# Kernel optimization log

Measured on AMD Instinct MI355X. Metric: run time of the kernel, lower is better.

The kernel has to match this reference:

```python
import jax, jax.numpy as jnp
import numpy as np

B = 65536          # number of 9-node graphs
NPG = 9            # nodes per graph (hardcoded in module)
N = B * NPG
D_IN, D_H = 11, 64
SOFTPLUS_BIAS = float(np.log(np.expm1(1.0)))  # biased_softplus_1.0 bias
SCALE_LB = 1e-4


def _make_edges():
    # fully connected (no self loops) within each 9-node graph
    pairs = np.array([(i, j) for i in range(NPG) for j in range(NPG) if i != j],
                     dtype=np.int64)  # [72, 2]
    offs = (np.arange(B, dtype=np.int64) * NPG)[:, None]
    src = (offs + pairs[None, :, 0]).ravel()
    dst = (offs + pairs[None, :, 1]).ravel()
    return jnp.asarray(np.stack([src, dst]))  # [2, E]


def setup_inputs() -> dict:
    key = jax.random.key(0)
    ks = jax.random.split(key, 12)
    s_in = 1.0 / np.sqrt(D_IN)
    s_h = 1.0 / np.sqrt(D_H)
    return {
        "x": jax.random.normal(ks[0], (N, D_IN), jnp.float32),
        "edge_index": _make_edges(),
        "W_in": jax.random.normal(ks[1], (D_H, D_IN), jnp.float32) * s_in,
        "b_in": jax.random.normal(ks[2], (D_H,), jnp.float32) * s_in,
        "W1_rel": jax.random.normal(ks[3], (D_H, D_H), jnp.float32) * s_h,
        "b1": jax.random.normal(ks[4], (D_H,), jnp.float32) * s_h,
        "W1_root": jax.random.normal(ks[5], (D_H, D_H), jnp.float32) * s_h,
        "W2_rel": jax.random.normal(ks[6], (D_H, D_H), jnp.float32) * s_h,
        "b2": jax.random.normal(ks[7], (D_H,), jnp.float32) * s_h,
        "W2_root": jax.random.normal(ks[8], (D_H, D_H), jnp.float32) * s_h,
        "W_head": jax.random.normal(ks[9], (8, D_H, 2), jnp.float32) * s_h,
        "b_head": jax.random.normal(ks[10], (8, 2), jnp.float32) * s_h,
    }


def _graph_conv(x, src, dst, W_rel, b_rel, W_root, n):
    # PyG GraphConv: lin_rel(sum_{j in N(i)} x_j) + lin_root(x_i)
    agg = jax.ops.segment_sum(x[src], dst, num_segments=n)  # scatter-add gather
    return agg @ W_rel.T + b_rel + x @ W_root.T


def reference(x, edge_index, W_in, b_in, W1_rel, b1, W1_root,
              W2_rel, b2, W2_root, W_head, b_head):
    n = x.shape[0]
    src, dst = edge_index[0], edge_index[1]
    h = x @ W_in.T + b_in                                   # [N, 64]
    h = jnp.tanh(_graph_conv(h, src, dst, W1_rel, b1, W1_root, n))
    h = jnp.tanh(_graph_conv(h, src, dst, W2_rel, b2, W2_root, n))
    hg = h.reshape(n // NPG, NPG, D_H)[:, 1:, :]            # drop node 0: [B, 8, 64]
    out = jnp.einsum('bnd,ndo->bno', hg, W_head) + b_head   # per-node head: [B, 8, 2]
    loc = out[..., 0]
    scale = jnp.maximum(jax.nn.softplus(out[..., 1] + SOFTPLUS_BIAS), SCALE_LB)
    return (loc, scale)
```

## Files before the change

### kernel.cpp

```cpp
#include <hip/hip_runtime.h>
#include <hip/hip_bf16.h>

#define NPG 9
#define DH 64
#define DIN 11
#define GPB 16
#define TPW 4
#define TPB 256
#define NGRAPH 65536
#define NBLK (NGRAPH/GPB)
#define XTOT (NGRAPH*NPG*DIN)
#define OUT_HALF ((long long)NGRAPH*8)

typedef __attribute__((ext_vector_type(8))) short short8;
typedef __attribute__((ext_vector_type(4))) float f32x4;

__device__ float g_c1[DH];
__device__ short g_bfrag1[8*512];
__device__ short g_bfrag2[16*512];
__device__ short g_bfragH[2*512];

__device__ __forceinline__ short f2bs(float f) {
  __hip_bfloat16 h = __float2bfloat16(f);
  return __builtin_bit_cast(short, h);
}
__device__ __forceinline__ float fast_tanh(float v) {
  float e = __expf(2.f*v);
  return 1.f - 2.f*__builtin_amdgcn_rcpf(e + 1.f);
}

__global__ void prep_kernel(const float* __restrict__ W_in, const float* __restrict__ b_in,
                            const float* __restrict__ W1_rel, const float* __restrict__ b1,
                            const float* __restrict__ W1_root,
                            const float* __restrict__ W2_rel, const float* __restrict__ W2_root,
                            const float* __restrict__ W_head) {
  const int blk = blockIdx.x, tid = threadIdx.x;
  if (blk < 2) {
    for (int i = blk*256 + tid; i < 8*512; i += 512) {
      int f = i >> 9, l = (i >> 3) & 63, j = i & 7;
      int k = ((l >> 4) << 3) + j;
      int n = ((f & 3) << 4) + (l & 15);
      float v = 0.f;
      if (k < DIN) {
        for (int m = 0; m < DH; ++m) {
          float wi = W_in[m*DIN + k];
          float r  = W1_rel[n*DH + m];
          v += ((f < 4) ? (W1_root[n*DH + m] - r) : r) * wi;
        }
      }
      g_bfrag1[i] = f2bs(v);
    }
  } else if (blk < 10) {
    for (int i = (blk - 2)*256 + tid; i < 16*512; i += 2048) {
      int frag = i >> 9, kk = frag >> 2;
      int l = (i >> 3) & 63, j = i & 7;
      int k2 = kk*32 + ((l >> 4) << 3) + j;
      int n  = (frag & 3)*16 + (l & 15);
      float v = (k2 < 64) ? (W2_root[n*DH + k2] - W2_rel[n*DH + k2])
                          : W2_rel[n*DH + k2 - 64];
      g_bfrag2[i] = f2bs(v);
    }
  } else if (blk == 10) {
    for (int i = tid; i < 2*512; i += 256) {
      int kk = i >> 9;
      int l = (i >> 3) & 63, j = i & 7;
      int k = kk*32 + ((l >> 4) << 3) + j;
      int n = l & 15;
      g_bfragH[i] = f2bs(W_head[(n >> 1)*(DH*2) + k*2 + (n & 1)]);
    }
  } else {
    if (tid < DH) {
      float c = b1[tid];
      for (int m = 0; m < DH; ++m)
        c += (W1_root[tid*DH + m] + 8.f*W1_rel[tid*DH + m]) * b_in[m];
      g_c1[tid] = c;
    }
  }
}

__global__ __launch_bounds__(TPB, 2) void fused_kernel(
    const float* __restrict__ x,
    const float* __restrict__ b2,
    const float* __restrict__ bhead,
    float* __restrict__ out)
{
  __shared__ short Hs[256*64];
  __shared__ short Ss[GPB*64];

  const int tid  = threadIdx.x;
  const int lane = tid & 63;
  const int wave = tid >> 6;
  const int l15  = lane & 15;
  const int kgrp = lane >> 4;
  const int ksel = kgrp & 1;
  const int t0   = wave*TPW;
  const unsigned gg0 = (unsigned)blockIdx.x*GPB + t0;

  {
    short8 By[4], Bu[4];
    #pragma unroll
    for (int nt = 0; nt < 4; ++nt) {
      By[nt] = *(const short8*)&g_bfrag1[nt*512 + lane*8];
      Bu[nt] = *(const short8*)&g_bfrag1[(4 + nt)*512 + lane*8];
    }
    float c1v[4];
    #pragma unroll
    for (int nt = 0; nt < 4; ++nt) c1v[nt] = g_c1[nt*16 + l15];

    float xr[TPW][8];
    #pragma unroll
    for (int i = 0; i < TPW; ++i) {
      const unsigned base = ((gg0 + i)*NPG + l15)*DIN + ksel*8;
      if (base + 8 <= (unsigned)XTOT) {
        #pragma unroll
        for (int j = 0; j < 8; ++j) xr[i][j] = x[base + j];
      } else {
        #pragma unroll
        for (int j = 0; j < 8; ++j) {
          const unsigned e = base + j;
          xr[i][j] = (e < (unsigned)XTOT) ? x[e] : 0.f;
        }
      }
    }

    const bool real = (l15 <= 8);
    #pragma unroll
    for (int i = 0; i < TPW; ++i) {
      const int T = t0 + i;
      short8 A;
      #pragma unroll
      for (int j = 0; j < 8; ++j) {
        bool ok = real && (ksel == 0 || j < 3);
        A[j] = ok ? f2bs(xr[i][j]) : (short)0;
      }
      f32x4 y[4], u[4];
      #pragma unroll
      for (int nt = 0; nt < 4; ++nt) { y[nt] = (f32x4){0,0,0,0}; u[nt] = (f32x4){0,0,0,0}; }
      #pragma unroll
      for (int nt = 0; nt < 4; ++nt) {
        y[nt] = __builtin_amdgcn_mfma_f32_16x16x32_bf16(A, By[nt], y[nt], 0, 0, 0);
        u[nt] = __builtin_amdgcn_mfma_f32_16x16x32_bf16(A, Bu[nt], u[nt], 0, 0, 0);
      }
      float suc[4];
      #pragma unroll
      for (int nt = 0; nt < 4; ++nt) {
        float s = (u[nt][0] + u[nt][1]) + (u[nt][2] + u[nt][3]);
        s += __shfl_xor(s, 16);
        s += __shfl_xor(s, 32);
        suc[nt] = s + c1v[nt];
      }
      float sh[4];
      #pragma unroll
      for (int nt = 0; nt < 4; ++nt) {
        float acc = 0.f;
        #pragma unroll
        for (int reg = 0; reg < 4; ++reg) {
          const int row = kgrp*4 + reg;
          float v = fast_tanh(y[nt][reg] + suc[nt]);
          v = (row <= 8) ? v : 0.f;
          acc += v;
          const int rr  = T*16 + row;
          const int col = nt*16 + l15;
          Hs[rr*64 + ((((col >> 3) ^ (row & 7))) << 3) + (col & 7)] = f2bs(v);
        }
        sh[nt] = acc;
      }
      #pragma unroll
      for (int nt = 0; nt < 4; ++nt) {
        float s = sh[nt];
        s += __shfl_xor(s, 16);
        s += __shfl_xor(s, 32);
        if (kgrp == 0) Ss[T*64 + nt*16 + l15] = f2bs(s);
      }
    }
  }

  {
    short8 B2[4][4];
    #pragma unroll
    for (int kk = 0; kk < 4; ++kk)
      #pragma unroll
      for (int nt = 0; nt < 4; ++nt)
        B2[kk][nt] = *(const short8*)&g_bfrag2[(kk*4 + nt)*512 + lane*8];
    float b2v[4];
    #pragma unroll
    for (int nt = 0; nt < 4; ++nt) b2v[nt] = b2[nt*16 + l15];

    #pragma unroll
    for (int i = 0; i < TPW; ++i) {
      const int T = t0 + i;
      const int row = T*16 + l15;
      short8 A0 = *(const short8*)&Hs[row*64 + (((0 + kgrp) ^ (l15 & 7)) << 3)];
      short8 A1 = *(const short8*)&Hs[row*64 + (((4 + kgrp) ^ (l15 & 7)) << 3)];
      short8 A2 = *(const short8*)&Ss[T*64 + kgrp*8];
      short8 A3 = *(const short8*)&Ss[T*64 + 32 + kgrp*8];
      f32x4 acc[4];
      #pragma unroll
      for (int nt = 0; nt < 4; ++nt)
        acc[nt] = (f32x4){b2v[nt], b2v[nt], b2v[nt], b2v[nt]};
      #pragma unroll
      for (int nt = 0; nt < 4; ++nt) {
        acc[nt] = __builtin_amdgcn_mfma_f32_16x16x32_bf16(A0, B2[0][nt], acc[nt], 0, 0, 0);
        acc[nt] = __builtin_amdgcn_mfma_f32_16x16x32_bf16(A1, B2[1][nt], acc[nt], 0, 0, 0);
        acc[nt] = __builtin_amdgcn_mfma_f32_16x16x32_bf16(A2, B2[2][nt], acc[nt], 0, 0, 0);
        acc[nt] = __builtin_amdgcn_mfma_f32_16x16x32_bf16(A3, B2[3][nt], acc[nt], 0, 0, 0);
      }
      #pragma unroll
      for (int nt = 0; nt < 4; ++nt) {
        #pragma unroll
        for (int reg = 0; reg < 4; ++reg) {
          const int row2 = kgrp*4 + reg;
          float v = fast_tanh(acc[nt][reg]);
          v = (row2 <= 8) ? v : 0.f;
          const int rr  = T*16 + row2;
          const int col = nt*16 + l15;
          Hs[rr*64 + ((((col >> 3) ^ (row2 & 7))) << 3) + (col & 7)] = f2bs(v);
        }
      }
    }
  }

  {
    short8 H0 = *(const short8*)&g_bfragH[lane*8];
    short8 H1 = *(const short8*)&g_bfragH[512 + lane*8];
    const int p  = l15 >> 1;
    const int oc = l15 & 1;
    const float bh = bhead[l15];
    const int trow = p + 1;
    const bool mykg = ((trow >> 2) == kgrp);
    const int treg = trow & 3;

    #pragma unroll
    for (int i = 0; i < TPW; ++i) {
      const int T = t0 + i;
      const int row = T*16 + l15;
      short8 A0 = *(const short8*)&Hs[row*64 + (((0 + kgrp) ^ (l15 & 7)) << 3)];
      short8 A1 = *(const short8*)&Hs[row*64 + (((4 + kgrp) ^ (l15 & 7)) << 3)];
      f32x4 acc = (f32x4){bh, bh, bh, bh};
      acc = __builtin_amdgcn_mfma_f32_16x16x32_bf16(A0, H0, acc, 0, 0, 0);
      acc = __builtin_amdgcn_mfma_f32_16x16x32_bf16(A1, H1, acc, 0, 0, 0);
      float val = (treg & 2) ? ((treg & 1) ? acc[3] : acc[2])
                             : ((treg & 1) ? acc[1] : acc[0]);
      float tv = val + 0.5413248546129181f;
      float e  = __expf(tv);
      float sp = (tv > 15.f) ? tv : __logf(1.f + e);
      sp = fmaxf(sp, 1e-4f);
      float res = oc ? sp : val;
      if (mykg) {
        const long long gg = (long long)blockIdx.x*GPB + T;
        out[(oc ? OUT_HALF : 0) + gg*8 + p] = res;
      }
    }
  }
}

extern "C" void kernel_launch(void* const* d_in, const int* in_sizes, int n_in,
                              void* d_out, int out_size, void* d_ws, size_t ws_size,
                              hipStream_t stream) {
  const float* x       = (const float*)d_in[0];
  const float* W_in    = (const float*)d_in[2];
  const float* b_in    = (const float*)d_in[3];
  const float* W1_rel  = (const float*)d_in[4];
  const float* b1      = (const float*)d_in[5];
  const float* W1_root = (const float*)d_in[6];
  const float* W2_rel  = (const float*)d_in[7];
  const float* b2      = (const float*)d_in[8];
  const float* W2_root = (const float*)d_in[9];
  const float* Whead   = (const float*)d_in[10];
  const float* bhead   = (const float*)d_in[11];
  float* out = (float*)d_out;

  hipLaunchKernelGGL(prep_kernel, dim3(12), dim3(256), 0, stream,
                     W_in, b_in, W1_rel, b1, W1_root, W2_rel, W2_root, Whead);
  hipLaunchKernelGGL(fused_kernel, dim3(NBLK), dim3(TPB), 0, stream,
                     x, b2, bhead, out);
}
```

Before: 214.2 us.

## Halve graphs per block, split layer-2 B fragments, raise occupancy, parallelize prep

Each block now handles 8 graphs instead of 16 (2 tiles per wave), which halves the shared-memory H buffer and raises the launch-bounds occupancy target from 2 to 3 blocks per CU. The layer-2 weight fragments are loaded in two halves, with accumulators kept live across all tiles, to cut register pressure. The prep kernel is spread over more blocks, stages weights through shared memory, and computes the bias reduction with a shuffle. In exchange there are twice as many blocks, each of which reloads the weight fragments, and more accumulator registers are live at once.

```diff
diff --git a/kernel.cpp b/kernel.cpp
--- a/kernel.cpp
+++ b/kernel.cpp
@@ -4,8 +4,8 @@
 #define NPG 9
 #define DH 64
 #define DIN 11
-#define GPB 16
-#define TPW 4
+#define GPB 8
+#define TPW 2
 #define TPB 256
 #define NGRAPH 65536
 #define NBLK (NGRAPH/GPB)
@@ -35,56 +35,71 @@
                             const float* __restrict__ W2_rel, const float* __restrict__ W2_root,
                             const float* __restrict__ W_head) {
   const int blk = blockIdx.x, tid = threadIdx.x;
-  if (blk < 2) {
-    for (int i = blk*256 + tid; i < 8*512; i += 512) {
-      int f = i >> 9, l = (i >> 3) & 63, j = i & 7;
-      int k = ((l >> 4) << 3) + j;
-      int n = ((f & 3) << 4) + (l & 15);
+  if (blk < 8) {
+    __shared__ float pw[704 + 4096 + 4096];
+    for (int i = tid; i < 704 + 4096 + 4096; i += TPB) {
+      float v;
+      if (i < 704)       v = W_in[i];
+      else if (i < 4800) v = W1_rel[i - 704];
+      else               v = W1_root[i - 4800];
+      pw[i] = v;
+    }
+    __syncthreads();
+    #pragma unroll
+    for (int e = 0; e < 2; ++e) {
+      const int i = blk*512 + e*256 + tid;
+      const int f = i >> 9, l = (i >> 3) & 63, j = i & 7;
+      const int k = ((l >> 4) << 3) + j;
+      const int n = ((f & 3) << 4) + (l & 15);
       float v = 0.f;
       if (k < DIN) {
+        const float* __restrict__ rel = &pw[704  + n*64];
+        const float* __restrict__ rt  = &pw[4800 + n*64];
         for (int m = 0; m < DH; ++m) {
-          float wi = W_in[m*DIN + k];
-          float r  = W1_rel[n*DH + m];
-          v += ((f < 4) ? (W1_root[n*DH + m] - r) : r) * wi;
+          float wi = pw[m*DIN + k];
+          v += ((f < 4) ? (rt[m] - rel[m]) : rel[m]) * wi;
         }
       }
       g_bfrag1[i] = f2bs(v);
     }
-  } else if (blk < 10) {
-    for (int i = (blk - 2)*256 + tid; i < 16*512; i += 2048) {
-      int frag = i >> 9, kk = frag >> 2;
-      int l = (i >> 3) & 63, j = i & 7;
-      int k2 = kk*32 + ((l >> 4) << 3) + j;
-      int n  = (frag & 3)*16 + (l & 15);
-      float v = (k2 < 64) ? (W2_root[n*DH + k2] - W2_rel[n*DH + k2])
-                          : W2_rel[n*DH + k2 - 64];
+  } else if (blk < 16) {
+    #pragma unroll
+    for (int e = 0; e < 4; ++e) {
+      const int i = (blk - 8)*1024 + e*256 + tid;
+      const int frag = i >> 9, kk = frag >> 2;
+      const int l = (i >> 3) & 63, j = i & 7;
+      const int k2 = kk*32 + ((l >> 4) << 3) + j;
+      const int n  = (frag & 3)*16 + (l & 15);
+      const float v = (k2 < 64) ? (W2_root[n*DH + k2] - W2_rel[n*DH + k2])
+                                : W2_rel[n*DH + k2 - 64];
       g_bfrag2[i] = f2bs(v);
     }
-  } else if (blk == 10) {
-    for (int i = tid; i < 2*512; i += 256) {
-      int kk = i >> 9;
-      int l = (i >> 3) & 63, j = i & 7;
-      int k = kk*32 + ((l >> 4) << 3) + j;
-      int n = l & 15;
+  } else if (blk == 16) {
+    for (int i = tid; i < 2*512; i += TPB) {
+      const int kk = i >> 9;
+      const int l = (i >> 3) & 63, j = i & 7;
+      const int k = kk*32 + ((l >> 4) << 3) + j;
+      const int n = l & 15;
       g_bfragH[i] = f2bs(W_head[(n >> 1)*(DH*2) + k*2 + (n & 1)]);
     }
   } else {
-    if (tid < DH) {
-      float c = b1[tid];
-      for (int m = 0; m < DH; ++m)
-        c += (W1_root[tid*DH + m] + 8.f*W1_rel[tid*DH + m]) * b_in[m];
-      g_c1[tid] = c;
-    }
+    const int n = tid >> 2, q = tid & 3;
+    float s = 0.f;
+    for (int m = q*16; m < q*16 + 16; ++m)
+      s += (W1_root[n*DH + m] + 8.f*W1_rel[n*DH + m]) * b_in[m];
+    s += __shfl_xor(s, 1);
+    s += __shfl_xor(s, 2);
+    if (q == 0) g_c1[n] = b1[n] + s;
   }
 }
 
-__global__ __launch_bounds__(TPB, 2) void fused_kernel(
+__global__ __launch_bounds__(TPB, 3) void fused_kernel(
     const float* __restrict__ x,
     const float* __restrict__ b2,
     const float* __restrict__ bhead,
     float* __restrict__ out)
 {
-  __shared__ short Hs[256*64];
+  __shared__ short Hs[128*64];
   __shared__ short Ss[GPB*64];
 
   const int tid  = threadIdx.x;
@@ -176,41 +191,53 @@
   }
 
   {
-    short8 B2[4][4];
-    #pragma unroll
-    for (int kk = 0; kk < 4; ++kk)
+    float b2v[4];
+    #pragma unroll
+    for (int nt = 0; nt < 4; ++nt) b2v[nt] = b2[nt*16 + l15];
+    f32x4 acc[TPW][4];
+    #pragma unroll
+    for (int i = 0; i < TPW; ++i)
       #pragma unroll
       for (int nt = 0; nt < 4; ++nt)
-        B2[kk][nt] = *(const short8*)&g_bfrag2[(kk*4 + nt)*512 + lane*8];
-    float b2v[4];
-    #pragma unroll
-    for (int nt = 0; nt < 4; ++nt) b2v[nt] = b2[nt*16 + l15];
+        acc[i][nt] = (f32x4){b2v[nt], b2v[nt], b2v[nt], b2v[nt]};
+
+    #pragma unroll
+    for (int h = 0; h < 2; ++h) {
+      short8 Bh[2][4];
+      #pragma unroll
+      for (int kk = 0; kk < 2; ++kk)
+        #pragma unroll
+        for (int nt = 0; nt < 4; ++nt)
+          Bh[kk][nt] = *(const short8*)&g_bfrag2[((h*2 + kk)*4 + nt)*512 + lane*8];
+      #pragma unroll
+      for (int i = 0; i < TPW; ++i) {
+        const int T = t0 + i;
+        short8 Aa, Ab;
+        if (h == 0) {
+          const int row = T*16 + l15;
+          Aa = *(const short8*)&Hs[row*64 + (((0 + kgrp) ^ (l15 & 7)) << 3)];
+          Ab = *(const short8*)&Hs[row*64 + (((4 + kgrp) ^ (l15 & 7)) << 3)];
+        } else {
+          Aa = *(const short8*)&Ss[T*64 + kgrp*8];
+          Ab = *(const short8*)&Ss[T*64 + 32 + kgrp*8];
+        }
+        #pragma unroll
+        for (int nt = 0; nt < 4; ++nt) {
+          acc[i][nt] = __builtin_amdgcn_mfma_f32_16x16x32_bf16(Aa, Bh[0][nt], acc[i][nt], 0, 0, 0);
+          acc[i][nt] = __builtin_amdgcn_mfma_f32_16x16x32_bf16(Ab, Bh[1][nt], acc[i][nt], 0, 0, 0);
+        }
+      }
+    }
 
     #pragma unroll
     for (int i = 0; i < TPW; ++i) {
       const int T = t0 + i;
-      const int row = T*16 + l15;
-      short8 A0 = *(const short8*)&Hs[row*64 + (((0 + kgrp) ^ (l15 & 7)) << 3)];
-      short8 A1 = *(const short8*)&Hs[row*64 + (((4 + kgrp) ^ (l15 & 7)) << 3)];
-      short8 A2 = *(const short8*)&Ss[T*64 + kgrp*8];
-      short8 A3 = *(const short8*)&Ss[T*64 + 32 + kgrp*8];
-      f32x4 acc[4];
-      #pragma unroll
-      for (int nt = 0; nt < 4; ++nt)
-        acc[nt] = (f32x4){b2v[nt], b2v[nt], b2v[nt], b2v[nt]};
-      #pragma unroll
-      for (int nt = 0; nt < 4; ++nt) {
-        acc[nt] = __builtin_amdgcn_mfma_f32_16x16x32_bf16(A0, B2[0][nt], acc[nt], 0, 0, 0);
-        acc[nt] = __builtin_amdgcn_mfma_f32_16x16x32_bf16(A1, B2[1][nt], acc[nt], 0, 0, 0);
-        acc[nt] = __builtin_amdgcn_mfma_f32_16x16x32_bf16(A2, B2[2][nt], acc[nt], 0, 0, 0);
-        acc[nt] = __builtin_amdgcn_mfma_f32_16x16x32_bf16(A3, B2[3][nt], acc[nt], 0, 0, 0);
-      }
       #pragma unroll
       for (int nt = 0; nt < 4; ++nt) {
         #pragma unroll
         for (int reg = 0; reg < 4; ++reg) {
           const int row2 = kgrp*4 + reg;
-          float v = fast_tanh(acc[nt][reg]);
+          float v = fast_tanh(acc[i][nt][reg]);
           v = (row2 <= 8) ? v : 0.f;
           const int rr  = T*16 + row2;
           const int col = nt*16 + l15;
@@ -270,7 +297,7 @@
   const float* bhead   = (const float*)d_in[11];
   float* out = (float*)d_out;
 
-  hipLaunchKernelGGL(prep_kernel, dim3(12), dim3(256), 0, stream,
+  hipLaunchKernelGGL(prep_kernel, dim3(18), dim3(TPB), 0, stream,
                      W_in, b_in, W1_rel, b1, W1_root, W2_rel, W2_root, Whead);
   hipLaunchKernelGGL(fused_kernel, dim3(NBLK), dim3(TPB), 0, stream,
                      x, b2, bhead, out);
```

Measured after the change: 182.7 us. 14.7% less time.
